# Performance work log

Hardware: AMD Instinct MI355X
Metric: run time of the kernel (lower is better)

Reference implementation:

```python
import jax, jax.numpy as jnp
import numpy as np


def setup_inputs() -> dict:
    key = jax.random.key(0)
    k1, k2 = jax.random.split(key)
    B, S, H, E = 4, 4096, 4096, 64
    hidden_states = jax.random.normal(k1, (B, S, H), dtype=jnp.float32)
    weight = jax.random.normal(k2, (E, H), dtype=jnp.float32) * 0.02
    return {"hidden_states": hidden_states, "weight": weight, "top_k": 8}


def reference(hidden_states, weight, top_k):
    # router logits: (B, S, E) = hidden @ weight.T, computed in fp32 as in torch path
    router_logits = jnp.einsum(
        "bsh,eh->bse",
        hidden_states.astype(jnp.float32),
        weight.astype(jnp.float32),
    )
    topk_weights, topk_indices = jax.lax.top_k(router_logits, top_k)
    topk_weights = jax.nn.softmax(topk_weights, axis=-1)
    return router_logits, topk_indices, topk_weights
```

## Files before the change

### kernel.cpp

```cpp
#include <hip/hip_runtime.h>
#include <math.h>

#define TOKENS 16384
#define HDIM   4096
#define NEXP   64
#define TOPK   8

#define BM 16
#define BK 32
#define LDF 36
#define CHUNKS (HDIM / BK)

typedef double f64x4 __attribute__((ext_vector_type(4)));

__global__ __launch_bounds__(256) void router_gemm_mfma(const float* __restrict__ hid,
                                                        const float* __restrict__ wgt,
                                                        float* __restrict__ logits) {
    __shared__ float As[2][BM * LDF];
    __shared__ float Bs[2][NEXP * LDF];

    const int tid  = threadIdx.x;
    const int bm   = blockIdx.x * BM;
    const int wv   = tid >> 6;
    const int lane = tid & 63;
    const int r    = lane & 15;
    const int kq   = lane >> 4;

    f64x4 rowp = {0., 0., 0., 0.};
    f64x4 colp = {0., 0., 0., 0.};
    rowp = __builtin_amdgcn_mfma_f64_16x16x4f64((double)r, 1.0, rowp, 0, 0, 0);
    colp = __builtin_amdgcn_mfma_f64_16x16x4f64(1.0, (double)r, colp, 0, 0, 0);
    int drow[4], dcol[4];
#pragma unroll
    for (int j = 0; j < 4; ++j) {
        drow[j] = (int)(rowp[j] * 0.25 + 0.5);
        dcol[j] = (int)(colp[j] * 0.25 + 0.5);
    }

    f64x4 acc = {0., 0., 0., 0.};

    const int arow = tid >> 3;
    const int af   = tid & 7;
    const int brow = tid >> 3;
    const int bf   = tid & 7;

    float4 pa0, pb00, pb10;
    float4 pa1, pb01, pb11;

#define LOAD_SET(PA, PB0, PB1, K0) do { \
        if (tid < 128) PA = *reinterpret_cast<const float4*>(&hid[(size_t)(bm + arow) * HDIM + (K0) + af * 4]); \
        PB0 = *reinterpret_cast<const float4*>(&wgt[(size_t)brow * HDIM + (K0) + bf * 4]); \
        PB1 = *reinterpret_cast<const float4*>(&wgt[(size_t)(brow + 32) * HDIM + (K0) + bf * 4]); \
    } while (0)

#define WRITE_SET(PA, PB0, PB1, BUF) do { \
        if (tid < 128) *reinterpret_cast<float4*>(&As[BUF][arow * LDF + af * 4]) = PA; \
        *reinterpret_cast<float4*>(&Bs[BUF][brow * LDF + bf * 4]) = PB0; \
        *reinterpret_cast<float4*>(&Bs[BUF][(brow + 32) * LDF + bf * 4]) = PB1; \
    } while (0)

#define COMPUTE(BUF) do { \
        const float* Ab = &As[BUF][r * LDF + kq]; \
        const float* Bb = &Bs[BUF][(wv * 16 + r) * LDF + kq]; \
        _Pragma("unroll") \
        for (int ks = 0; ks < 8; ++ks) { \
            acc = __builtin_amdgcn_mfma_f64_16x16x4f64((double)Ab[ks * 4], (double)Bb[ks * 4], acc, 0, 0, 0); \
        } \
    } while (0)

    LOAD_SET(pa0, pb00, pb10, 0);
    WRITE_SET(pa0, pb00, pb10, 0);
    LOAD_SET(pa1, pb01, pb11, BK);

    for (int c = 0; c < CHUNKS; c += 2) {
        __syncthreads();
        if (c + 2 < CHUNKS) LOAD_SET(pa0, pb00, pb10, (c + 2) * BK);
        COMPUTE(0);
        WRITE_SET(pa1, pb01, pb11, 1);
        __syncthreads();
        if (c + 3 < CHUNKS) LOAD_SET(pa1, pb01, pb11, (c + 3) * BK);
        COMPUTE(1);
        if (c + 2 < CHUNKS) WRITE_SET(pa0, pb00, pb10, 0);
    }

#undef LOAD_SET
#undef WRITE_SET
#undef COMPUTE

#pragma unroll
    for (int j = 0; j < 4; ++j) {
        const int row = bm + drow[j];
        const int col = wv * 16 + dcol[j];
        logits[(size_t)row * NEXP + col] = (float)acc[j];
    }
}

__global__ __launch_bounds__(256) void topk_softmax(const float* __restrict__ logits,
                                                    float* __restrict__ out_idx,
                                                    float* __restrict__ out_w) {
    const int wave  = threadIdx.x >> 6;
    const int lane  = threadIdx.x & 63;
    const int token = blockIdx.x * 4 + wave;
    if (token >= TOKENS) return;

    float v = logits[(size_t)token * NEXP + lane];

    float myval = 0.f;
    int   myidx = 0;
    float max0  = 0.f;

#pragma unroll
    for (int k = 0; k < TOPK; ++k) {
        float bv = v;
        int   bi = lane;
#pragma unroll
        for (int off = 32; off > 0; off >>= 1) {
            float ov = __shfl_xor(bv, off);
            int   oi = __shfl_xor(bi, off);
            if (ov > bv || (ov == bv && oi < bi)) { bv = ov; bi = oi; }
        }
        if (k == 0) max0 = bv;
        if (lane == k) { myval = bv; myidx = bi; }
        if (lane == bi) v = -INFINITY;
    }

    float e = (lane < TOPK) ? expf(myval - max0) : 0.f;
    float s = e;
#pragma unroll
    for (int off = 4; off > 0; off >>= 1) s += __shfl_xor(s, off);

    if (lane < TOPK) {
        size_t o = (size_t)token * TOPK + lane;
        out_idx[o] = (float)myidx;
        out_w[o]   = e / s;
    }
}

extern "C" void kernel_launch(void* const* d_in, const int* in_sizes, int n_in,
                              void* d_out, int out_size, void* d_ws, size_t ws_size,
                              hipStream_t stream) {
    const float* hid = (const float*)d_in[0];
    const float* wgt = (const float*)d_in[1];

    float* logits  = (float*)d_out;
    float* out_idx = logits + (size_t)TOKENS * NEXP;
    float* out_w   = out_idx + (size_t)TOKENS * TOPK;

    router_gemm_mfma<<<TOKENS / BM, 256, 0, stream>>>(hid, wgt, logits);
    topk_softmax<<<TOKENS / 4, 256, 0, stream>>>(logits, out_idx, out_w);
}
```

Before: 188.1 us.

## Double K-tile to 64 with XOR-swizzled shared memory and single-stage prefetch

Raises the K chunk from 32 to 64, which halves the number of barrier-separated iterations and gives all threads a hidden-state load. The padded shared-memory layout is replaced by an XOR swizzle on 4-float groups to avoid bank conflicts without padding. The two-deep register prefetch becomes a single prefetch with ping-pong buffers. This removes one level of prefetch depth and adds shared memory per block, which may reduce occupancy or latency hiding.

```diff
diff --git a/kernel.cpp b/kernel.cpp
--- a/kernel.cpp
+++ b/kernel.cpp
@@ -7,8 +7,7 @@
 #define TOPK   8
 
 #define BM 16
-#define BK 32
-#define LDF 36
+#define BK 64
 #define CHUNKS (HDIM / BK)
 
 typedef double f64x4 __attribute__((ext_vector_type(4)));
@@ -16,8 +15,8 @@
 __global__ __launch_bounds__(256) void router_gemm_mfma(const float* __restrict__ hid,
                                                         const float* __restrict__ wgt,
                                                         float* __restrict__ logits) {
-    __shared__ float As[2][BM * LDF];
-    __shared__ float Bs[2][NEXP * LDF];
+    __shared__ float As[2][BM * BK];
+    __shared__ float Bs[2][NEXP * BK];
 
     const int tid  = threadIdx.x;
     const int bm   = blockIdx.x * BM;
@@ -25,6 +24,7 @@
     const int lane = tid & 63;
     const int r    = lane & 15;
     const int kq   = lane >> 4;
+    const int swz  = r & 7;
 
     f64x4 rowp = {0., 0., 0., 0.};
     f64x4 colp = {0., 0., 0., 0.};
@@ -39,48 +39,47 @@
 
     f64x4 acc = {0., 0., 0., 0.};
 
-    const int arow = tid >> 3;
-    const int af   = tid & 7;
-    const int brow = tid >> 3;
-    const int bf   = tid & 7;
+    const int arow = tid >> 4;
+    const int af   = tid & 15;
+    const int brow = tid >> 2;
+    const int bf   = tid & 3;
 
-    float4 pa0, pb00, pb10;
-    float4 pa1, pb01, pb11;
+    float4 pa, pb[4];
 
-#define LOAD_SET(PA, PB0, PB1, K0) do { \
-        if (tid < 128) PA = *reinterpret_cast<const float4*>(&hid[(size_t)(bm + arow) * HDIM + (K0) + af * 4]); \
-        PB0 = *reinterpret_cast<const float4*>(&wgt[(size_t)brow * HDIM + (K0) + bf * 4]); \
-        PB1 = *reinterpret_cast<const float4*>(&wgt[(size_t)(brow + 32) * HDIM + (K0) + bf * 4]); \
+#define LOAD_SET(K0) do { \
+        pa = *reinterpret_cast<const float4*>(&hid[(size_t)(bm + arow) * HDIM + (K0) + af * 4]); \
+        _Pragma("unroll") \
+        for (int j = 0; j < 4; ++j) \
+            pb[j] = *reinterpret_cast<const float4*>(&wgt[(size_t)brow * HDIM + (K0) + (bf + 4 * j) * 4]); \
     } while (0)
 
-#define WRITE_SET(PA, PB0, PB1, BUF) do { \
-        if (tid < 128) *reinterpret_cast<float4*>(&As[BUF][arow * LDF + af * 4]) = PA; \
-        *reinterpret_cast<float4*>(&Bs[BUF][brow * LDF + bf * 4]) = PB0; \
-        *reinterpret_cast<float4*>(&Bs[BUF][(brow + 32) * LDF + bf * 4]) = PB1; \
+#define WRITE_SET(BUF) do { \
+        *reinterpret_cast<float4*>(&As[BUF][arow * BK + ((af * 4) ^ ((arow & 7) << 2))]) = pa; \
+        _Pragma("unroll") \
+        for (int j = 0; j < 4; ++j) \
+            *reinterpret_cast<float4*>(&Bs[BUF][brow * BK + (((bf + 4 * j) * 4) ^ ((brow & 7) << 2))]) = pb[j]; \
     } while (0)
 
 #define COMPUTE(BUF) do { \
-        const float* Ab = &As[BUF][r * LDF + kq]; \
-        const float* Bb = &Bs[BUF][(wv * 16 + r) * LDF + kq]; \
+        const float* Ab = &As[BUF][r * BK + kq]; \
+        const float* Bb = &Bs[BUF][(wv * 16 + r) * BK + kq]; \
         _Pragma("unroll") \
-        for (int ks = 0; ks < 8; ++ks) { \
-            acc = __builtin_amdgcn_mfma_f64_16x16x4f64((double)Ab[ks * 4], (double)Bb[ks * 4], acc, 0, 0, 0); \
+        for (int ks = 0; ks < 16; ++ks) { \
+            const int o = 4 * (ks ^ swz); \
+            acc = __builtin_amdgcn_mfma_f64_16x16x4f64((double)Ab[o], (double)Bb[o], acc, 0, 0, 0); \
         } \
     } while (0)
 
-    LOAD_SET(pa0, pb00, pb10, 0);
-    WRITE_SET(pa0, pb00, pb10, 0);
-    LOAD_SET(pa1, pb01, pb11, BK);
+    LOAD_SET(0);
+    WRITE_SET(0);
 
-    for (int c = 0; c < CHUNKS; c += 2) {
+    int cur = 0;
+    for (int c = 0; c < CHUNKS; ++c) {
         __syncthreads();
-        if (c + 2 < CHUNKS) LOAD_SET(pa0, pb00, pb10, (c + 2) * BK);
-        COMPUTE(0);
-        WRITE_SET(pa1, pb01, pb11, 1);
-        __syncthreads();
-        if (c + 3 < CHUNKS) LOAD_SET(pa1, pb01, pb11, (c + 3) * BK);
-        COMPUTE(1);
-        if (c + 2 < CHUNKS) WRITE_SET(pa0, pb00, pb10, 0);
+        if (c + 1 < CHUNKS) LOAD_SET((c + 1) * BK);
+        COMPUTE(cur);
+        if (c + 1 < CHUNKS) WRITE_SET(cur ^ 1);
+        cur ^= 1;
     }
 
 #undef LOAD_SET
```

Measured after the change: 202.8 us. 7.8% more time.
